# Kernel optimization log

Measured on AMD Instinct MI355X. Metric: run time of the kernel, lower is better.

Reference implementation:

```python
import jax, jax.numpy as jnp
import numpy as np

B, S, D, H, E, TOP_K = 8, 2048, 2048, 2048, 4, 2


def setup_inputs() -> dict:
    key = jax.random.key(0)
    ks = jax.random.split(key, 6)
    scale = 0.02
    return {
        "hidden_states": jax.random.normal(ks[0], (B, S, D), jnp.float32),
        "gate_w": jax.random.normal(ks[1], (E, D), jnp.float32) * scale,  # Linear(D -> E), no bias
        "w1": jax.random.normal(ks[2], (E, D, H), jnp.float32) * scale,   # per-expert Linear(D -> H)
        "b1": jnp.zeros((E, H), jnp.float32),
        "w2": jax.random.normal(ks[3], (E, H, H), jnp.float32) * scale,   # per-expert Linear(H -> H)
        "b2": jnp.zeros((E, H), jnp.float32),
    }


def reference(hidden_states, gate_w, w1, b1, w2, b2):
    b, s, d = hidden_states.shape
    x = hidden_states.reshape(-1, d)                       # [N, D]
    n = x.shape[0]

    # Router: softmax in fp32, top-k, renormalize (matches torch forward)
    logits = jnp.einsum("nd,ed->ne", x, gate_w)            # [N, E]
    rw = jax.nn.softmax(logits.astype(jnp.float32), axis=-1)
    top_w, sel = jax.lax.top_k(rw, TOP_K)                  # [N, K]
    top_w = top_w / jnp.sum(top_w, axis=-1, keepdims=True)
    top_w = top_w.astype(x.dtype)

    # Scatter top-k weights back to a dense [N, E] combine matrix
    w_full = jnp.zeros((n, E), x.dtype).at[jnp.arange(n)[:, None], sel].set(top_w)

    # Per-expert FFN: Linear -> exact GELU -> Linear (dense over all tokens,
    # combined with zero weight for unselected experts == gather/scatter math)
    h1 = jax.nn.gelu(jnp.einsum("nd,edh->enh", x, w1) + b1[:, None, :], approximate=False)
    out_e = jnp.einsum("enh,eho->eno", h1, w2) + b2[:, None, :]  # [E, N, H]

    out = jnp.einsum("eno,ne->no", out_e, w_full)          # weighted combine
    return out.reshape(b, s, -1)
```

## Files before the change

kernel.cpp:

```cpp
#include <hip/hip_runtime.h>
#include <hip/hip_bf16.h>
#include <math.h>

typedef __bf16 bf16x8 __attribute__((ext_vector_type(8)));
typedef __bf16 bf16x4 __attribute__((ext_vector_type(4)));
typedef float f32x4 __attribute__((ext_vector_type(4)));

typedef __attribute__((address_space(1))) void GV;
typedef __attribute__((address_space(3))) void LV;

template <int OSTRIDE, bool EBLOCK>
__global__ __launch_bounds__(256) void transpose_cvt(const float* __restrict__ in,
                                                     __bf16* __restrict__ out) {
  __shared__ float tile[32][33];
  const int e = blockIdx.z;
  const size_t ibase = (size_t)e * 2048 * 2048;
  const size_t obase = EBLOCK ? (size_t)e * 2048 * 2048 : (size_t)e * 2048;
  int c0 = blockIdx.x * 32, r0 = blockIdx.y * 32;
  int tx = threadIdx.x & 31, ty = threadIdx.x >> 5;
#pragma unroll
  for (int i = 0; i < 32; i += 8)
    tile[ty + i][tx] = in[ibase + (size_t)(r0 + ty + i) * 2048 + c0 + tx];
  __syncthreads();
#pragma unroll
  for (int i = 0; i < 32; i += 8)
    out[obase + (size_t)(c0 + ty + i) * OSTRIDE + r0 + tx] = (__bf16)tile[tx][ty + i];
}

__global__ __launch_bounds__(256) void router_fused(const float4* __restrict__ hs4,
                                                    const float4* __restrict__ gw4,
                                                    bf16x4* __restrict__ xb,
                                                    float* __restrict__ comb,
                                                    int* __restrict__ pairid,
                                                    int* __restrict__ cnt) {
  __shared__ float4 gwS[4 * 512];
  const int tid = threadIdx.x;
  for (int j = tid; j < 2048; j += 256) gwS[j] = gw4[j];
  __syncthreads();

  const int lane = tid & 63;
  const int wv = tid >> 6;
  const int nA = blockIdx.x * 8 + wv * 2;
  const int nB = nA + 1;

  const float4* xA = hs4 + (size_t)nA * 512;
  const float4* xB = hs4 + (size_t)nB * 512;
  bf16x4* dA = xb + (size_t)nA * 512;
  bf16x4* dB = xb + (size_t)nB * 512;

  float4 va[8], vb[8];
#pragma unroll
  for (int i = 0; i < 8; ++i) va[i] = xA[i * 64 + lane];
#pragma unroll
  for (int i = 0; i < 8; ++i) vb[i] = xB[i * 64 + lane];

  float a0 = 0.f, a1 = 0.f, a2 = 0.f, a3 = 0.f;
  float c0 = 0.f, c1 = 0.f, c2 = 0.f, c3 = 0.f;
#pragma unroll
  for (int i = 0; i < 8; ++i) {
    int j = i * 64 + lane;
    float4 g0 = gwS[j], g1 = gwS[512 + j], g2 = gwS[1024 + j], g3 = gwS[1536 + j];
    float4 v = va[i];
    a0 += v.x * g0.x + v.y * g0.y + v.z * g0.z + v.w * g0.w;
    a1 += v.x * g1.x + v.y * g1.y + v.z * g1.z + v.w * g1.w;
    a2 += v.x * g2.x + v.y * g2.y + v.z * g2.z + v.w * g2.w;
    a3 += v.x * g3.x + v.y * g3.y + v.z * g3.z + v.w * g3.w;
    bf16x4 oa;
    oa.x = (__bf16)v.x; oa.y = (__bf16)v.y; oa.z = (__bf16)v.z; oa.w = (__bf16)v.w;
    dA[j] = oa;
    float4 w = vb[i];
    c0 += w.x * g0.x + w.y * g0.y + w.z * g0.z + w.w * g0.w;
    c1 += w.x * g1.x + w.y * g1.y + w.z * g1.z + w.w * g1.w;
    c2 += w.x * g2.x + w.y * g2.y + w.z * g2.z + w.w * g2.w;
    c3 += w.x * g3.x + w.y * g3.y + w.z * g3.z + w.w * g3.w;
    bf16x4 ob;
    ob.x = (__bf16)w.x; ob.y = (__bf16)w.y; ob.z = (__bf16)w.z; ob.w = (__bf16)w.w;
    dB[j] = ob;
  }

#pragma unroll
  for (int off = 32; off > 0; off >>= 1) {
    a0 += __shfl_xor(a0, off); a1 += __shfl_xor(a1, off);
    a2 += __shfl_xor(a2, off); a3 += __shfl_xor(a3, off);
    c0 += __shfl_xor(c0, off); c1 += __shfl_xor(c1, off);
    c2 += __shfl_xor(c2, off); c3 += __shfl_xor(c3, off);
  }

  if (lane < 2) {
    const int n = lane ? nB : nA;
    float l[4];
    l[0] = lane ? c0 : a0; l[1] = lane ? c1 : a1;
    l[2] = lane ? c2 : a2; l[3] = lane ? c3 : a3;
    float m = fmaxf(fmaxf(l[0], l[1]), fmaxf(l[2], l[3]));
    float p[4], sum = 0.f;
#pragma unroll
    for (int e = 0; e < 4; ++e) { p[e] = expf(l[e] - m); sum += p[e]; }
#pragma unroll
    for (int e = 0; e < 4; ++e) p[e] /= sum;
    int i1 = 0;
#pragma unroll
    for (int e = 1; e < 4; ++e) if (p[e] > p[i1]) i1 = e;
    int i2 = -1;
#pragma unroll
    for (int e = 0; e < 4; ++e) {
      if (e == i1) continue;
      if (i2 < 0 || p[e] > p[i2]) i2 = e;
    }
    float ws = p[i1] + p[i2];
#pragma unroll
    for (int e = 0; e < 4; ++e)
      comb[(size_t)n * 4 + e] = (e == i1 || e == i2) ? p[e] / ws : 0.f;
    int a = min(i1, i2), b = max(i1, i2);
    int pid = (a == 0) ? (b - 1) : ((a == 1) ? (1 + b) : (2 + b));
    pairid[n] = pid;
    atomicAdd(&cnt[pid], 1);
  }
}

__global__ void scan6(const int* __restrict__ cnt, int* __restrict__ off) {
  int o = 0;
  for (int i = 0; i < 6; ++i) { off[i] = o; o += cnt[i]; }
}

__global__ __launch_bounds__(256) void assign_kernel(const int* __restrict__ pairid,
                                                     const float4* __restrict__ comb4,
                                                     const int* __restrict__ off,
                                                     int* __restrict__ cur,
                                                     int* __restrict__ perm,
                                                     float4* __restrict__ comb_s,
                                                     int* __restrict__ pm_s) {
  int n = blockIdx.x * 256 + threadIdx.x;
  int pid = pairid[n];
  int pos = off[pid] + atomicAdd(&cur[pid], 1);
  perm[pos] = n;
  comb_s[pos] = comb4[n];
  const int lut[6] = {3, 5, 9, 6, 10, 12};
  pm_s[pos] = lut[pid];
}

__global__ void tile_mask_kernel(const int* __restrict__ pm_s, int* __restrict__ tmask) {
  int t = threadIdx.x;
  int m = 0;
  for (int i = 0; i < 256; ++i) m |= pm_s[t * 256 + i];
  tmask[t] = m;
}

template <int MODE>
__global__ __launch_bounds__(512) void gemm256(const __bf16* __restrict__ A,
                                               const __bf16* __restrict__ Bt,
                                               const float* __restrict__ bias,
                                               const float* __restrict__ cc,
                                               const int* __restrict__ tmask,
                                               const int* __restrict__ permc,
                                               void* __restrict__ outp) {
  constexpr int K = (MODE == 0) ? 2048 : 8192;
  __shared__ __attribute__((aligned(128))) __bf16 lds[65536];

  const int tid = threadIdx.x;
  const int lane = tid & 63, wv = tid >> 6;
  const int wm = wv >> 2, wn = wv & 3;
  const int lrow = lane & 15, quad = lane >> 4;
  const int bx = blockIdx.x, by = blockIdx.y;

  const int tm = tmask[by];
  if (MODE == 0 && !(tm & (1 << (bx >> 3)))) return;

  int nt, aep = 0;
  if (MODE == 0) {
    nt = K / 64;
  } else {
    int na = 0;
    for (int e = 0; e < 4; ++e)
      if (tm & (1 << e)) { aep |= e << (na * 8); ++na; }
    nt = na * 32;
  }
  auto kb_of = [&](int t) -> int {
    return (MODE == 0) ? t : ((aep >> ((t >> 5) * 8)) & 7) * 32 + (t & 31);
  };

  const __bf16* asrc[4];
  const __bf16* bsrc[4];
  int lofA[4], lofB[4];
#pragma unroll
  for (int i = 0; i < 4; ++i) {
    int c = i * 512 + tid;
    int row = c >> 3, cc8 = (c & 7) ^ (row & 7);
    int arow = by * 256 + row;
    if (MODE == 0) arow = permc[arow];
    asrc[i] = A + (size_t)arow * K + cc8 * 8;
    bsrc[i] = Bt + (size_t)(bx * 256 + row) * K + cc8 * 8;
    lofA[i] = (i * 512 + wv * 64) * 8;
    lofB[i] = 32768 + (i * 512 + wv * 64) * 8;
  }

  auto stageA = [&](int nbuf, int kb) {
#pragma unroll
    for (int i = 0; i < 4; ++i)
      __builtin_amdgcn_global_load_lds((GV*)(asrc[i] + (size_t)kb * 64),
                                       (LV*)&lds[nbuf * 16384 + lofA[i]], 16, 0, 0);
  };
  auto stageB = [&](int nbuf, int kb) {
#pragma unroll
    for (int i = 0; i < 4; ++i)
      __builtin_amdgcn_global_load_lds((GV*)(bsrc[i] + (size_t)kb * 64),
                                       (LV*)&lds[nbuf * 16384 + lofB[i]], 16, 0, 0);
  };

  const int aoff = wm * 8192 + lrow * 64;
  const int boff = wn * 4096 + lrow * 64;
  const int sk0 = (quad ^ (lrow & 7)) * 8;
  const int sk1 = ((4 + quad) ^ (lrow & 7)) * 8;

  f32x4 acc[8][4] = {};
  bf16x8 af[4][2];
  bf16x8 bfr[2][2][2];

#define LDA_FRAGS(MH)                                                          \
  _Pragma("unroll") for (int m = 0; m < 4; ++m) {                              \
    af[m][0] = *(const bf16x8*)&lds[cb16 + aoff + (MH)*4096 + m * 1024 + sk0]; \
    af[m][1] = *(const bf16x8*)&lds[cb16 + aoff + (MH)*4096 + m * 1024 + sk1]; \
  }
#define LDB_FRAGS(NH)                                                          \
  _Pragma("unroll") for (int n = 0; n < 2; ++n) {                              \
    bfr[NH][n][0] =                                                            \
        *(const bf16x8*)&lds[32768 + cb16 + boff + (NH)*2048 + n * 1024 + sk0];\
    bfr[NH][n][1] =                                                            \
        *(const bf16x8*)&lds[32768 + cb16 + boff + (NH)*2048 + n * 1024 + sk1];\
  }
#define BARRIER_LGKM                                                           \
  __builtin_amdgcn_s_barrier();                                                \
  asm volatile("s_waitcnt lgkmcnt(0)" ::: "memory");                           \
  __builtin_amdgcn_sched_barrier(0);
#define MFMA_Q(MH, NH)                                                         \
  __builtin_amdgcn_s_setprio(1);                                               \
  _Pragma("unroll") for (int m = 0; m < 4; ++m)                                \
      _Pragma("unroll") for (int n = 0; n < 2; ++n) {                          \
    acc[(MH)*4 + m][(NH)*2 + n] = __builtin_amdgcn_mfma_f32_16x16x32_bf16(     \
        af[m][0], bfr[NH][n][0], acc[(MH)*4 + m][(NH)*2 + n], 0, 0, 0);        \
    acc[(MH)*4 + m][(NH)*2 + n] = __builtin_amdgcn_mfma_f32_16x16x32_bf16(     \
        af[m][1], bfr[NH][n][1], acc[(MH)*4 + m][(NH)*2 + n], 0, 0, 0);        \
  }                                                                            \
  __builtin_amdgcn_s_setprio(0);

  {
    int kb0 = kb_of(0);
    stageA(0, kb0);
    stageB(0, kb0);
  }
  asm volatile("s_waitcnt vmcnt(0)" ::: "memory");
  __builtin_amdgcn_s_barrier();

  for (int t = 0; t < nt; ++t) {
    const int cb16 = (t & 1) * 16384;
    const int nbuf = (t & 1) ^ 1;
    const bool more = (t + 1) < nt;
    const int kbn = more ? kb_of(t + 1) : 0;

    LDA_FRAGS(0)
    LDB_FRAGS(0)
    if (more) stageA(nbuf, kbn);
    BARRIER_LGKM
    MFMA_Q(0, 0)
    __builtin_amdgcn_s_barrier();

    LDB_FRAGS(1)
    if (more) stageB(nbuf, kbn);
    BARRIER_LGKM
    MFMA_Q(0, 1)
    __builtin_amdgcn_s_barrier();

    LDA_FRAGS(1)
    BARRIER_LGKM
    MFMA_Q(1, 1)
    __builtin_amdgcn_s_barrier();

    BARRIER_LGKM
    MFMA_Q(1, 0)
    asm volatile("s_waitcnt vmcnt(0)" ::: "memory");
    __builtin_amdgcn_s_barrier();
  }

#undef LDA_FRAGS
#undef LDB_FRAGS
#undef BARRIER_LGKM
#undef MFMA_Q

  if (MODE == 0) {
    __bf16* out = (__bf16*)outp;
#pragma unroll
    for (int mq = 0; mq < 8; ++mq) {
#pragma unroll
      for (int nq = 0; nq < 4; ++nq) {
        int gcol = bx * 256 + wn * 64 + nq * 16 + lrow;
        int e = gcol >> 11;
        int h = gcol & 2047;
        float b = bias[e * 2048 + h];
        f32x4 v = acc[mq][nq];
#pragma unroll
        for (int r = 0; r < 4; ++r) {
          int row = by * 256 + wm * 128 + mq * 16 + quad * 4 + r;
          float xv = v[r] + b;
          float gl = 0.5f * xv * (1.0f + erff(xv * 0.70710678118654752440f));
          out[(size_t)row * 8192 + gcol] = (__bf16)(gl * cc[row * 4 + e]);
        }
      }
    }
  } else {
    float* out = (float*)outp;
    float bb[4][4];
#pragma unroll
    for (int nq = 0; nq < 4; ++nq) {
      int gcol = bx * 256 + wn * 64 + nq * 16 + lrow;
#pragma unroll
      for (int e = 0; e < 4; ++e) bb[nq][e] = bias[e * 2048 + gcol];
    }
#pragma unroll
    for (int mq = 0; mq < 8; ++mq) {
#pragma unroll
      for (int r = 0; r < 4; ++r) {
        int row = by * 256 + wm * 128 + mq * 16 + quad * 4 + r;
        int tok = permc[row];
        const float* cw = cc + (size_t)row * 4;
        float c0 = cw[0], c1 = cw[1], c2 = cw[2], c3 = cw[3];
#pragma unroll
        for (int nq = 0; nq < 4; ++nq) {
          int gcol = bx * 256 + wn * 64 + nq * 16 + lrow;
          float s = acc[mq][nq][r] + c0 * bb[nq][0] + c1 * bb[nq][1] +
                    c2 * bb[nq][2] + c3 * bb[nq][3];
          out[(size_t)tok * 2048 + gcol] = s;
        }
      }
    }
  }
}

extern "C" void kernel_launch(void* const* d_in, const int* in_sizes, int n_in,
                              void* d_out, int out_size, void* d_ws, size_t ws_size,
                              hipStream_t stream) {
  const float* hs = (const float*)d_in[0];
  const float* gate_w = (const float*)d_in[1];
  const float* w1 = (const float*)d_in[2];
  const float* b1 = (const float*)d_in[3];
  const float* w2 = (const float*)d_in[4];
  const float* b2 = (const float*)d_in[5];
  float* out = (float*)d_out;

  const int N = 16384, D = 2048, H = 2048, E = 4;

  char* p = (char*)d_ws;
  __bf16* xb = (__bf16*)p;    p += (size_t)N * D * 2;
  __bf16* w1t = (__bf16*)p;   p += (size_t)E * D * H * 2;
  __bf16* w2t = (__bf16*)p;   p += (size_t)E * H * H * 2;
  float* comb = (float*)p;    p += (size_t)N * 4 * 4;
  float* comb_s = (float*)p;  p += (size_t)N * 4 * 4;
  int* perm = (int*)p;        p += (size_t)N * 4;
  int* pairid = (int*)p;      p += (size_t)N * 4;
  int* pm_s = (int*)p;        p += (size_t)N * 4;
  int* meta = (int*)p;        p += 32 * 4;
  int* tmask = (int*)p;       p += 64 * 4;
  __bf16* h1s = (__bf16*)p;

  size_t used = (size_t)(p - (char*)d_ws);
  int CHUNK = 4096;
  if (ws_size >= used + (size_t)16384 * 8192 * 2) CHUNK = 16384;
  else if (ws_size >= used + (size_t)8192 * 8192 * 2) CHUNK = 8192;

  hipMemsetAsync(meta, 0, 64, stream);
  transpose_cvt<2048, true><<<dim3(64, 64, 4), 256, 0, stream>>>(w1, w1t);
  transpose_cvt<8192, false><<<dim3(64, 64, 4), 256, 0, stream>>>(w2, w2t);
  router_fused<<<dim3(N / 8), 256, 0, stream>>>((const float4*)hs,
                                                (const float4*)gate_w,
                                                (bf16x4*)xb, comb, pairid, meta);
  scan6<<<1, 1, 0, stream>>>(meta, meta + 16);
  assign_kernel<<<dim3(N / 256), 256, 0, stream>>>(pairid, (const float4*)comb,
                                                   meta + 16, meta + 8, perm,
                                                   (float4*)comb_s, pm_s);
  tile_mask_kernel<<<1, 64, 0, stream>>>(pm_s, tmask);

  for (int c = 0; c < N / CHUNK; ++c) {
    const float* cc = comb_s + (size_t)c * CHUNK * 4;
    const int* tmc = tmask + c * (CHUNK / 256);
    gemm256<0><<<dim3(E * H / 256, CHUNK / 256), 512, 0, stream>>>(
        xb, w1t, b1, cc, tmc, perm + c * CHUNK, h1s);
    gemm256<1><<<dim3(H / 256, CHUNK / 256), 512, 0, stream>>>(
        h1s, w2t, b2, cc, tmc, perm + c * CHUNK, out);
  }
}
```

Baseline: 1.441 ms.

## Switch GEMM main loop to 4-stage K=32 pipeline with deeper prefetch

The 256x256 GEMM main loop changes from a double-buffered K=64 tile with four barrier-separated quarter phases to a four-buffer ring of K=32 tiles. It keeps three stages in flight and uses graded vmcnt waits. Each step now loads all fragments at once and issues 32 MFMAs with a single barrier per step, which is meant to hide global latency better and cut barrier count per FLOP. In exchange, the LDS layout drops the XOR swizzle, so fragment reads with a 64-byte row stride may hit bank conflicts, and loop overhead per K element doubles.

```diff
diff --git a/kernel.cpp b/kernel.cpp
--- a/kernel.cpp
+++ b/kernel.cpp
@@ -154,7 +154,7 @@
                                                const int* __restrict__ permc,
                                                void* __restrict__ outp) {
   constexpr int K = (MODE == 0) ? 2048 : 8192;
-  __shared__ __attribute__((aligned(128))) __bf16 lds[65536];
+  __shared__ __attribute__((aligned(128))) __bf16 lds[4 * 16384];
 
   const int tid = threadIdx.x;
   const int lane = tid & 63, wv = tid >> 6;
@@ -167,123 +167,86 @@
 
   int nt, aep = 0;
   if (MODE == 0) {
-    nt = K / 64;
+    nt = K / 32;
   } else {
     int na = 0;
     for (int e = 0; e < 4; ++e)
       if (tm & (1 << e)) { aep |= e << (na * 8); ++na; }
-    nt = na * 32;
-  }
-  auto kb_of = [&](int t) -> int {
-    return (MODE == 0) ? t : ((aep >> ((t >> 5) * 8)) & 7) * 32 + (t & 31);
+    nt = na * 64;
+  }
+  auto kb_of = [&](int s) -> int {
+    return (MODE == 0) ? s : ((aep >> ((s >> 6) * 8)) & 7) * 64 + (s & 63);
   };
 
-  const __bf16* asrc[4];
-  const __bf16* bsrc[4];
-  int lofA[4], lofB[4];
-#pragma unroll
-  for (int i = 0; i < 4; ++i) {
+  const __bf16* asrc[2];
+  const __bf16* bsrc[2];
+  int lofA[2], lofB[2];
+#pragma unroll
+  for (int i = 0; i < 2; ++i) {
     int c = i * 512 + tid;
-    int row = c >> 3, cc8 = (c & 7) ^ (row & 7);
+    int row = c >> 2, kc = c & 3;
     int arow = by * 256 + row;
     if (MODE == 0) arow = permc[arow];
-    asrc[i] = A + (size_t)arow * K + cc8 * 8;
-    bsrc[i] = Bt + (size_t)(bx * 256 + row) * K + cc8 * 8;
+    asrc[i] = A + (size_t)arow * K + kc * 8;
+    bsrc[i] = Bt + (size_t)(bx * 256 + row) * K + kc * 8;
     lofA[i] = (i * 512 + wv * 64) * 8;
-    lofB[i] = 32768 + (i * 512 + wv * 64) * 8;
-  }
-
-  auto stageA = [&](int nbuf, int kb) {
-#pragma unroll
-    for (int i = 0; i < 4; ++i)
-      __builtin_amdgcn_global_load_lds((GV*)(asrc[i] + (size_t)kb * 64),
-                                       (LV*)&lds[nbuf * 16384 + lofA[i]], 16, 0, 0);
+    lofB[i] = 8192 + (i * 512 + wv * 64) * 8;
+  }
+
+  auto stage = [&](int s) {
+    const int b = (s & 3) * 16384;
+    const int kb = kb_of(s);
+#pragma unroll
+    for (int i = 0; i < 2; ++i) {
+      __builtin_amdgcn_global_load_lds((GV*)(asrc[i] + (size_t)kb * 32),
+                                       (LV*)&lds[b + lofA[i]], 16, 0, 0);
+      __builtin_amdgcn_global_load_lds((GV*)(bsrc[i] + (size_t)kb * 32),
+                                       (LV*)&lds[b + lofB[i]], 16, 0, 0);
+    }
   };
-  auto stageB = [&](int nbuf, int kb) {
-#pragma unroll
-    for (int i = 0; i < 4; ++i)
-      __builtin_amdgcn_global_load_lds((GV*)(bsrc[i] + (size_t)kb * 64),
-                                       (LV*)&lds[nbuf * 16384 + lofB[i]], 16, 0, 0);
-  };
-
-  const int aoff = wm * 8192 + lrow * 64;
-  const int boff = wn * 4096 + lrow * 64;
-  const int sk0 = (quad ^ (lrow & 7)) * 8;
-  const int sk1 = ((4 + quad) ^ (lrow & 7)) * 8;
 
   f32x4 acc[8][4] = {};
-  bf16x8 af[4][2];
-  bf16x8 bfr[2][2][2];
-
-#define LDA_FRAGS(MH)                                                          \
-  _Pragma("unroll") for (int m = 0; m < 4; ++m) {                              \
-    af[m][0] = *(const bf16x8*)&lds[cb16 + aoff + (MH)*4096 + m * 1024 + sk0]; \
-    af[m][1] = *(const bf16x8*)&lds[cb16 + aoff + (MH)*4096 + m * 1024 + sk1]; \
-  }
-#define LDB_FRAGS(NH)                                                          \
-  _Pragma("unroll") for (int n = 0; n < 2; ++n) {                              \
-    bfr[NH][n][0] =                                                            \
-        *(const bf16x8*)&lds[32768 + cb16 + boff + (NH)*2048 + n * 1024 + sk0];\
-    bfr[NH][n][1] =                                                            \
-        *(const bf16x8*)&lds[32768 + cb16 + boff + (NH)*2048 + n * 1024 + sk1];\
-  }
-#define BARRIER_LGKM                                                           \
-  __builtin_amdgcn_s_barrier();                                                \
-  asm volatile("s_waitcnt lgkmcnt(0)" ::: "memory");                           \
-  __builtin_amdgcn_sched_barrier(0);
-#define MFMA_Q(MH, NH)                                                         \
-  __builtin_amdgcn_s_setprio(1);                                               \
-  _Pragma("unroll") for (int m = 0; m < 4; ++m)                                \
-      _Pragma("unroll") for (int n = 0; n < 2; ++n) {                          \
-    acc[(MH)*4 + m][(NH)*2 + n] = __builtin_amdgcn_mfma_f32_16x16x32_bf16(     \
-        af[m][0], bfr[NH][n][0], acc[(MH)*4 + m][(NH)*2 + n], 0, 0, 0);        \
-    acc[(MH)*4 + m][(NH)*2 + n] = __builtin_amdgcn_mfma_f32_16x16x32_bf16(     \
-        af[m][1], bfr[NH][n][1], acc[(MH)*4 + m][(NH)*2 + n], 0, 0, 0);        \
-  }                                                                            \
-  __builtin_amdgcn_s_setprio(0);
-
-  {
-    int kb0 = kb_of(0);
-    stageA(0, kb0);
-    stageB(0, kb0);
-  }
-  asm volatile("s_waitcnt vmcnt(0)" ::: "memory");
+
+  stage(0);
+  stage(1);
+  stage(2);
+  asm volatile("s_waitcnt vmcnt(8)" ::: "memory");
   __builtin_amdgcn_s_barrier();
 
-  for (int t = 0; t < nt; ++t) {
-    const int cb16 = (t & 1) * 16384;
-    const int nbuf = (t & 1) ^ 1;
-    const bool more = (t + 1) < nt;
-    const int kbn = more ? kb_of(t + 1) : 0;
-
-    LDA_FRAGS(0)
-    LDB_FRAGS(0)
-    if (more) stageA(nbuf, kbn);
-    BARRIER_LGKM
-    MFMA_Q(0, 0)
+  for (int s = 0; s < nt; ++s) {
+    const int b = (s & 3) * 16384;
+
+    bf16x8 af[8], bfr[4];
+#pragma unroll
+    for (int m = 0; m < 8; ++m)
+      af[m] = *(const bf16x8*)&lds[b + (wm * 128 + m * 16 + lrow) * 32 + quad * 8];
+#pragma unroll
+    for (int n = 0; n < 4; ++n)
+      bfr[n] = *(const bf16x8*)&lds[b + 8192 + (wn * 64 + n * 16 + lrow) * 32 + quad * 8];
+
+    if (s + 3 < nt) stage(s + 3);
+
+    asm volatile("s_waitcnt lgkmcnt(0)" ::: "memory");
+    __builtin_amdgcn_sched_barrier(0);
+
+    __builtin_amdgcn_s_setprio(1);
+#pragma unroll
+    for (int m = 0; m < 8; ++m)
+#pragma unroll
+      for (int n = 0; n < 4; ++n)
+        acc[m][n] =
+            __builtin_amdgcn_mfma_f32_16x16x32_bf16(af[m], bfr[n], acc[m][n], 0, 0, 0);
+    __builtin_amdgcn_s_setprio(0);
+
+    const int rem = nt - 1 - s;
+    if (rem >= 3)
+      asm volatile("s_waitcnt vmcnt(8)" ::: "memory");
+    else if (rem == 2)
+      asm volatile("s_waitcnt vmcnt(4)" ::: "memory");
+    else if (rem == 1)
+      asm volatile("s_waitcnt vmcnt(0)" ::: "memory");
     __builtin_amdgcn_s_barrier();
-
-    LDB_FRAGS(1)
-    if (more) stageB(nbuf, kbn);
-    BARRIER_LGKM
-    MFMA_Q(0, 1)
-    __builtin_amdgcn_s_barrier();
-
-    LDA_FRAGS(1)
-    BARRIER_LGKM
-    MFMA_Q(1, 1)
-    __builtin_amdgcn_s_barrier();
-
-    BARRIER_LGKM
-    MFMA_Q(1, 0)
-    asm volatile("s_waitcnt vmcnt(0)" ::: "memory");
-    __builtin_amdgcn_s_barrier();
-  }
-
-#undef LDA_FRAGS
-#undef LDB_FRAGS
-#undef BARRIER_LGKM
-#undef MFMA_Q
+  }
 
   if (MODE == 0) {
     __bf16* out = (__bf16*)outp;
```

Measured after the change: 1.449 ms. About the same (+0.6%).
